# Kernel tuning notes

Hardware: AMD Instinct MI355X
Metric: run time of the kernel (lower is better)

## Reference

```python
import jax, jax.numpy as jnp
import numpy as np

HEADS = 4
DIM_HEAD = 64


def setup_inputs() -> dict:
    key = jax.random.key(0)
    k1, k2, k3, k4 = jax.random.split(key, 4)
    dim = 256
    hidden = HEADS * DIM_HEAD  # 256
    x = jax.random.normal(k1, (16, dim, 64, 64), dtype=jnp.float32)
    # 1x1 conv weights stored as [out_c, in_c]
    w_qkv = jax.random.normal(k2, (3 * hidden, dim), dtype=jnp.float32) * (1.0 / np.sqrt(dim))
    w_out = jax.random.normal(k3, (dim, hidden), dtype=jnp.float32) * (1.0 / np.sqrt(hidden))
    b_out = jax.random.normal(k4, (dim,), dtype=jnp.float32) * 0.01
    gamma = jnp.ones((dim,), dtype=jnp.float32) * 1e-05
    return {"x": x, "w_qkv": w_qkv, "w_out": w_out, "b_out": b_out, "gamma": gamma}


def reference(x, w_qkv, w_out, b_out, gamma):
    b, c, h, w = x.shape
    n = h * w
    # 1x1 conv == channel matmul
    qkv = jnp.einsum('oc,bchw->bohw', w_qkv, x)  # [b, 3*heads*dh, h, w]
    qkv = qkv.reshape(b, 3, HEADS, DIM_HEAD, n)  # channel split order: (qkv, heads, c)
    q, k, v = qkv[:, 0], qkv[:, 1], qkv[:, 2]    # each [b, heads, dh, n]
    k = jax.nn.softmax(k, axis=-1)               # softmax over spatial tokens
    context = jnp.einsum('bhdn,bhen->bhde', k, v)  # [b, heads, dh, dh]
    out = jnp.einsum('bhde,bhdn->bhen', context, q)  # [b, heads, dh, n]
    out = out.reshape(b, HEADS * DIM_HEAD, h, w)
    y = jnp.einsum('oc,bchw->bohw', w_out, out) + b_out[None, :, None, None]
    return y * gamma[None, :, None, None] + x
```

## Files before the change

kernel.cpp:

```cpp
#include <hip/hip_runtime.h>
#include <stdint.h>

typedef short s16x8 __attribute__((ext_vector_type(8)));
typedef float f32x4 __attribute__((ext_vector_type(4)));

__device__ __forceinline__ float bits2f(unsigned short u) {
    union { unsigned int i; float f; } c; c.i = ((unsigned int)u) << 16; return c.f;
}
__device__ __forceinline__ unsigned short f2bits(float f) {
    union { float f; unsigned int i; } c; c.f = f;
    unsigned int x = c.i;
    unsigned int r = (x + 0x7FFFu + ((x >> 16) & 1u)) >> 16;
    return (unsigned short)r;
}
__device__ __forceinline__ unsigned int pack2(float a, float b) {
    return (unsigned int)f2bits(a) | ((unsigned int)f2bits(b) << 16);
}

__global__ __launch_bounds__(256) void k_cvt(
    const float* __restrict__ src, unsigned short* __restrict__ dst, int n8)
{
    int i = blockIdx.x * 256 + threadIdx.x;
    if (i >= n8) return;
    const float* s = src + (size_t)i * 8;
    float4 a = *(const float4*)s, b = *(const float4*)(s + 4);
    unsigned int q[4] = { pack2(a.x, a.y), pack2(a.z, a.w), pack2(b.x, b.y), pack2(b.z, b.w) };
    *(s16x8*)(dst + (size_t)i * 8) = *(s16x8*)q;
}

__global__ __launch_bounds__(256) void k_transpose(
    const unsigned short* __restrict__ src, unsigned short* __restrict__ dst,
    int RS, int DS)
{
    int dr = blockIdx.x * 256 + threadIdx.x;
    int c0 = blockIdx.y * 8;
    __align__(16) unsigned short tmp[8];
#pragma unroll
    for (int j = 0; j < 8; ++j) tmp[j] = src[(size_t)(c0 + j) * RS + dr];
    *(s16x8*)(dst + (size_t)dr * DS + c0) = *(s16x8*)tmp;
}

template <int BF32>
__global__ __launch_bounds__(256) void gemm_bt(
    const unsigned short* __restrict__ A, const void* __restrict__ Bt,
    unsigned short* __restrict__ C,
    int K, int Kstep, int lda, int ldb, int ldc,
    long Abs, long Bbs, long Cbs)
{
    __shared__ unsigned short As[128][72];
    __shared__ unsigned short Bs[128][72];
    int bz = blockIdx.z;
    int b = bz & 15, kc = bz >> 4;
    int m0 = blockIdx.y * 128, n0 = blockIdx.x * 128;
    const unsigned short* Ab = A + (size_t)b * Abs + (size_t)m0 * lda + (size_t)kc * Kstep;
    size_t boff = (size_t)b * Bbs + (size_t)n0 * ldb + (size_t)kc * Kstep;
    int t = threadIdx.x;
    int w = t >> 6, l = t & 63, lm = l & 15, lq = l >> 4;
    int mw = (w >> 1) * 64, nw = (w & 1) * 64;

    f32x4 acc[4][4];
    f32x4 zero = {0.f, 0.f, 0.f, 0.f};
#pragma unroll
    for (int i = 0; i < 4; ++i)
#pragma unroll
        for (int j = 0; j < 4; ++j) acc[i][j] = zero;

    for (int kk = 0; kk < K; kk += 64) {
#pragma unroll
        for (int i = 0; i < 4; ++i) {
            int idx = t + i * 256;
            int r = idx >> 3, ch = idx & 7;
            *(s16x8*)&As[r][ch * 8] = *(const s16x8*)(Ab + (size_t)r * lda + kk + ch * 8);
            if (BF32) {
                const float* bp = (const float*)Bt + boff + (size_t)r * ldb + kk + ch * 8;
                float4 v0 = *(const float4*)bp, v1 = *(const float4*)(bp + 4);
                unsigned int q[4] = { pack2(v0.x, v0.y), pack2(v0.z, v0.w),
                                      pack2(v1.x, v1.y), pack2(v1.z, v1.w) };
                *(s16x8*)&Bs[r][ch * 8] = *(s16x8*)q;
            } else {
                const unsigned short* bp = (const unsigned short*)Bt + boff + (size_t)r * ldb + kk + ch * 8;
                *(s16x8*)&Bs[r][ch * 8] = *(const s16x8*)bp;
            }
        }
        __syncthreads();
#pragma unroll
        for (int ks = 0; ks < 2; ++ks) {
            s16x8 af[4], bfr[4];
#pragma unroll
            for (int mi = 0; mi < 4; ++mi) af[mi]  = *(const s16x8*)&As[mw + mi * 16 + lm][ks * 32 + lq * 8];
#pragma unroll
            for (int ni = 0; ni < 4; ++ni) bfr[ni] = *(const s16x8*)&Bs[nw + ni * 16 + lm][ks * 32 + lq * 8];
#pragma unroll
            for (int mi = 0; mi < 4; ++mi)
#pragma unroll
                for (int ni = 0; ni < 4; ++ni)
                    acc[mi][ni] = __builtin_amdgcn_mfma_f32_16x16x32_bf16(af[mi], bfr[ni], acc[mi][ni], 0, 0, 0);
        }
        __syncthreads();
    }

    unsigned short* Cb = C + (size_t)bz * Cbs;
#pragma unroll
    for (int mi = 0; mi < 4; ++mi)
#pragma unroll
        for (int r = 0; r < 4; ++r) {
            int m = m0 + mw + mi * 16 + lq * 4 + r;
#pragma unroll
            for (int ni = 0; ni < 4; ++ni) {
                int n = n0 + nw + ni * 16 + lm;
                Cb[(size_t)m * ldc + n] = f2bits(acc[mi][ni][r]);
            }
        }
}

template <int EPI>
__global__ __launch_bounds__(256) void gemm_bn(
    const unsigned short* __restrict__ A, const float* __restrict__ B,
    void* __restrict__ C,
    int K, int lda, int ldb, int ldc,
    long Abs, long Bbs, long Cbs,
    const float* __restrict__ Xres,
    const float* __restrict__ gamma,
    const float* __restrict__ bias)
{
    __shared__ unsigned short As[128][72];
    __shared__ unsigned short Bs[64][130];
    int bz = blockIdx.z;
    int m0 = blockIdx.y * 128, n0 = blockIdx.x * 128;
    const unsigned short* Ab = A + (size_t)bz * Abs + (size_t)m0 * lda;
    const float* Bb = B + (size_t)bz * Bbs + n0;
    int t = threadIdx.x;
    int w = t >> 6, l = t & 63, lm = l & 15, lq = l >> 4;
    int mw = (w >> 1) * 64, nw = (w & 1) * 64;

    f32x4 acc[4][4];
    f32x4 zero = {0.f, 0.f, 0.f, 0.f};
#pragma unroll
    for (int i = 0; i < 4; ++i)
#pragma unroll
        for (int j = 0; j < 4; ++j) acc[i][j] = zero;

    for (int kk = 0; kk < K; kk += 64) {
#pragma unroll
        for (int i = 0; i < 4; ++i) {
            int idx = t + i * 256;
            int r = idx >> 3, ch = idx & 7;
            *(s16x8*)&As[r][ch * 8] = *(const s16x8*)(Ab + (size_t)r * lda + kk + ch * 8);
        }
#pragma unroll
        for (int i = 0; i < 4; ++i) {
            int idx = t + i * 256;
            int c = idx >> 4, cc = idx & 15;
            const float* bp = Bb + (size_t)(kk + c) * ldb + cc * 8;
            float4 v0 = *(const float4*)bp, v1 = *(const float4*)(bp + 4);
            unsigned int* q = (unsigned int*)&Bs[c][cc * 8];
            q[0] = pack2(v0.x, v0.y); q[1] = pack2(v0.z, v0.w);
            q[2] = pack2(v1.x, v1.y); q[3] = pack2(v1.z, v1.w);
        }
        __syncthreads();
#pragma unroll
        for (int ks = 0; ks < 2; ++ks) {
            s16x8 af[4];
#pragma unroll
            for (int mi = 0; mi < 4; ++mi) af[mi] = *(const s16x8*)&As[mw + mi * 16 + lm][ks * 32 + lq * 8];
#pragma unroll
            for (int ni = 0; ni < 4; ++ni) {
                s16x8 bfr;
#pragma unroll
                for (int j = 0; j < 8; ++j) bfr[j] = (short)Bs[ks * 32 + lq * 8 + j][nw + ni * 16 + lm];
#pragma unroll
                for (int mi = 0; mi < 4; ++mi)
                    acc[mi][ni] = __builtin_amdgcn_mfma_f32_16x16x32_bf16(af[mi], bfr, acc[mi][ni], 0, 0, 0);
            }
        }
        __syncthreads();
    }

#pragma unroll
    for (int mi = 0; mi < 4; ++mi)
#pragma unroll
        for (int r = 0; r < 4; ++r) {
            int m = m0 + mw + mi * 16 + lq * 4 + r;
            float g = 0.f, bo = 0.f;
            if (EPI == 1) { g = gamma[m]; bo = bias[m]; }
#pragma unroll
            for (int ni = 0; ni < 4; ++ni) {
                int n = n0 + nw + ni * 16 + lm;
                size_t idx = (size_t)m * ldc + n;
                float v = acc[mi][ni][r];
                if (EPI == 1) {
                    float* Cb = (float*)C + (size_t)bz * Cbs;
                    Cb[idx] = g * (v + bo) + Xres[(size_t)bz * Cbs + idx];
                } else {
                    unsigned short* Cb = (unsigned short*)C + (size_t)bz * Cbs;
                    Cb[idx] = f2bits(v);
                }
            }
        }
}

__global__ __launch_bounds__(256) void k_softmax(unsigned short* __restrict__ kbuf)
{
    unsigned short* p = kbuf + (size_t)blockIdx.x * 4096;
    int t = threadIdx.x;
    __shared__ float red[4];

    s16x8 r0 = *(const s16x8*)(p + t * 16);
    s16x8 r1 = *(const s16x8*)(p + t * 16 + 8);
    float v[16];
    float m = -1e30f;
#pragma unroll
    for (int i = 0; i < 8; ++i) { v[i] = bits2f((unsigned short)r0[i]); v[8 + i] = bits2f((unsigned short)r1[i]); }
#pragma unroll
    for (int i = 0; i < 16; ++i) m = fmaxf(m, v[i]);
#pragma unroll
    for (int off = 32; off >= 1; off >>= 1) m = fmaxf(m, __shfl_xor(m, off));
    if ((t & 63) == 0) red[t >> 6] = m;
    __syncthreads();
    m = fmaxf(fmaxf(red[0], red[1]), fmaxf(red[2], red[3]));
    __syncthreads();

    float s = 0.f;
#pragma unroll
    for (int i = 0; i < 16; ++i) { v[i] = __expf(v[i] - m); s += v[i]; }
#pragma unroll
    for (int off = 32; off >= 1; off >>= 1) s += __shfl_xor(s, off);
    if ((t & 63) == 0) red[t >> 6] = s;
    __syncthreads();
    s = red[0] + red[1] + red[2] + red[3];
    float inv = 1.0f / s;

    __align__(16) unsigned short otmp[16];
#pragma unroll
    for (int i = 0; i < 16; ++i) otmp[i] = f2bits(v[i] * inv);
    *(s16x8*)(p + t * 16) = *(s16x8*)(otmp);
    *(s16x8*)(p + t * 16 + 8) = *(s16x8*)(otmp + 8);
}

__global__ __launch_bounds__(256) void k_gred(
    const unsigned short* __restrict__ Gp, unsigned short* __restrict__ G)
{
    int gid = blockIdx.x * 256 + threadIdx.x;
    int b = gid >> 13;
    size_t i8 = (size_t)(gid & 8191) * 8;
    float s[8] = {0.f, 0.f, 0.f, 0.f, 0.f, 0.f, 0.f, 0.f};
#pragma unroll
    for (int kc = 0; kc < 8; ++kc) {
        s16x8 v = *(const s16x8*)(Gp + (size_t)(kc * 16 + b) * 65536 + i8);
#pragma unroll
        for (int j = 0; j < 8; ++j) s[j] += bits2f((unsigned short)v[j]);
    }
    __align__(16) unsigned short tmp[8];
#pragma unroll
    for (int j = 0; j < 8; ++j) tmp[j] = f2bits(s[j]);
    *(s16x8*)(G + (size_t)b * 65536 + i8) = *(s16x8*)tmp;
}

__global__ __launch_bounds__(256) void k_ctxw2(
    const unsigned short* __restrict__ G, const unsigned short* __restrict__ wb,
    const unsigned short* __restrict__ wob, unsigned short* __restrict__ W2)
{
    __shared__ unsigned short ctxs[64][72];
    int h = blockIdx.x, b = blockIdx.y;
    int t = threadIdx.x, w = t >> 6, l = t & 63, lm = l & 15, lq = l >> 4;
    const unsigned short* Gb = G + (size_t)b * 65536 + (size_t)(h * 64) * 256;
    const unsigned short* Wv = wb + 131072 + (size_t)(h * 64) * 256;
    f32x4 zero = {0.f, 0.f, 0.f, 0.f};

    f32x4 acc[4];
#pragma unroll
    for (int i = 0; i < 4; ++i) acc[i] = zero;
    for (int kk = 0; kk < 256; kk += 32) {
        s16x8 a = *(const s16x8*)(Gb + (size_t)(w * 16 + lm) * 256 + kk + lq * 8);
#pragma unroll
        for (int ni = 0; ni < 4; ++ni) {
            s16x8 bb = *(const s16x8*)(Wv + (size_t)(ni * 16 + lm) * 256 + kk + lq * 8);
            acc[ni] = __builtin_amdgcn_mfma_f32_16x16x32_bf16(a, bb, acc[ni], 0, 0, 0);
        }
    }
#pragma unroll
    for (int ni = 0; ni < 4; ++ni)
#pragma unroll
        for (int r = 0; r < 4; ++r)
            ctxs[w * 16 + lq * 4 + r][ni * 16 + lm] = f2bits(acc[ni][r]);
    __syncthreads();

    f32x4 acc2[4][4];
#pragma unroll
    for (int i = 0; i < 4; ++i)
#pragma unroll
        for (int j = 0; j < 4; ++j) acc2[i][j] = zero;
#pragma unroll
    for (int ks = 0; ks < 2; ++ks) {
        s16x8 af[4], bfr[4];
#pragma unroll
        for (int mi = 0; mi < 4; ++mi)
            af[mi] = *(const s16x8*)(wob + (size_t)(w * 64 + mi * 16 + lm) * 256 + h * 64 + ks * 32 + lq * 8);
#pragma unroll
        for (int ni = 0; ni < 4; ++ni) bfr[ni] = *(const s16x8*)&ctxs[ni * 16 + lm][ks * 32 + lq * 8];
#pragma unroll
        for (int mi = 0; mi < 4; ++mi)
#pragma unroll
            for (int ni = 0; ni < 4; ++ni)
                acc2[mi][ni] = __builtin_amdgcn_mfma_f32_16x16x32_bf16(af[mi], bfr[ni], acc2[mi][ni], 0, 0, 0);
    }
    unsigned short* W2b = W2 + (size_t)b * 65536;
#pragma unroll
    for (int mi = 0; mi < 4; ++mi)
#pragma unroll
        for (int r = 0; r < 4; ++r) {
            int o = w * 64 + mi * 16 + lq * 4 + r;
#pragma unroll
            for (int ni = 0; ni < 4; ++ni)
                W2b[(size_t)o * 256 + h * 64 + ni * 16 + lm] = f2bits(acc2[mi][ni][r]);
        }
}

extern "C" void kernel_launch(void* const* d_in, const int* in_sizes, int n_in,
                              void* d_out, int out_size, void* d_ws, size_t ws_size,
                              hipStream_t stream)
{
    (void)in_sizes; (void)n_in; (void)out_size; (void)ws_size;
    const float* x      = (const float*)d_in[0];
    const float* w_qkv  = (const float*)d_in[1];
    const float* w_out  = (const float*)d_in[2];
    const float* b_out  = (const float*)d_in[3];
    const float* gamma  = (const float*)d_in[4];
    unsigned short* kbuf = (unsigned short*)d_out;

    char* ws = (char*)d_ws;
    unsigned short* Gp  = (unsigned short*)(ws);
    unsigned short* G   = (unsigned short*)(ws + 16777216);
    unsigned short* W2  = (unsigned short*)(ws + 18874368);
    unsigned short* W3  = (unsigned short*)(ws + 20971520);
    unsigned short* WqT = (unsigned short*)(ws + 23068672);
    unsigned short* wb  = (unsigned short*)(ws + 23199744);
    unsigned short* wob = (unsigned short*)(ws + 23592960);

    k_cvt<<<dim3(96), 256, 0, stream>>>(w_qkv, wb, 24576);
    k_cvt<<<dim3(32), 256, 0, stream>>>(w_out, wob, 8192);

    k_transpose<<<dim3(1, 32, 1), 256, 0, stream>>>(wb, WqT, 256, 256);

    gemm_bn<0><<<dim3(32, 2, 16), 256, 0, stream>>>(
        wb + 65536, x, kbuf, 256, 256, 4096, 4096,
        0L, 1048576L, 1048576L, nullptr, nullptr, nullptr);

    k_softmax<<<dim3(4096), 256, 0, stream>>>(kbuf);

    gemm_bt<1><<<dim3(2, 2, 128), 256, 0, stream>>>(
        kbuf, x, Gp, 512, 512, 4096, 4096, 256,
        1048576L, 1048576L, 65536L);

    k_gred<<<dim3(512), 256, 0, stream>>>(Gp, G);

    k_ctxw2<<<dim3(4, 16), 256, 0, stream>>>(G, wb, wob, W2);

    gemm_bt<0><<<dim3(2, 2, 16), 256, 0, stream>>>(
        W2, WqT, W3, 256, 0, 256, 256, 256,
        65536L, 0L, 65536L);

    gemm_bn<1><<<dim3(32, 2, 16), 256, 0, stream>>>(
        W3, x, d_out, 256, 256, 4096, 4096,
        65536L, 1048576L, 1048576L, x, gamma, b_out);
}
```

Baseline: 228.7 us.

## Pre-transpose x to bf16 token-major and route big GEMMs through gemm_bt

Adds a prep kernel that converts x to bf16 and transposes it to [n][c] layout in workspace. The K-projection GEMM and the final output GEMM, which has a fused bias, gamma and residual epilogue, now use the B-transposed bf16 GEMM path instead of the fp32 row-major path. The three weight-prep kernels are merged into one launch. Gp moves into the upper half of d_out. This trades an extra 32 MB bf16 write and read of x for cheaper, conversion-free operand loads in two GEMMs, and it depends on a workspace size check, falling back to the old path when the workspace is too small.

```diff
diff --git a/kernel.cpp b/kernel.cpp
--- a/kernel.cpp
+++ b/kernel.cpp
@@ -40,12 +40,68 @@
     *(s16x8*)(dst + (size_t)dr * DS + c0) = *(s16x8*)tmp;
 }
 
-template <int BF32>
+__global__ __launch_bounds__(256) void k_prepw(
+    const float* __restrict__ wqkv, const float* __restrict__ wout,
+    unsigned short* __restrict__ wb, unsigned short* __restrict__ wob,
+    unsigned short* __restrict__ WqT)
+{
+    int i = blockIdx.x * 256 + threadIdx.x;
+    if (i < 32768) {
+        const float* s; unsigned short* d; int j;
+        if (i < 24576) { s = wqkv; d = wb; j = i; }
+        else           { s = wout; d = wob; j = i - 24576; }
+        const float* sp = s + (size_t)j * 8;
+        float4 a = *(const float4*)sp, b = *(const float4*)(sp + 4);
+        unsigned int q[4] = { pack2(a.x, a.y), pack2(a.z, a.w), pack2(b.x, b.y), pack2(b.z, b.w) };
+        *(s16x8*)(d + (size_t)j * 8) = *(s16x8*)q;
+    } else {
+        int j = i - 32768;
+        int dr = j & 255, c0 = (j >> 8) * 8;
+        __align__(16) unsigned short tmp[8];
+#pragma unroll
+        for (int jj = 0; jj < 8; ++jj)
+            tmp[jj] = f2bits(wqkv[(size_t)(c0 + jj) * 256 + dr]);
+        *(s16x8*)(WqT + (size_t)dr * 256 + c0) = *(s16x8*)tmp;
+    }
+}
+
+__global__ __launch_bounds__(256) void k_prep(
+    const float* __restrict__ x, unsigned short* __restrict__ xT)
+{
+    __shared__ unsigned short Ts[64][264];
+    int b = blockIdx.y, n0 = blockIdx.x * 64, t = threadIdx.x;
+    const float* xb = x + (size_t)b * 1048576;
+#pragma unroll
+    for (int i = 0; i < 16; ++i) {
+        int idx = t + i * 256;
+        int c = idx >> 4, nq = idx & 15;
+        float4 v = *(const float4*)(xb + (size_t)c * 4096 + n0 + nq * 4);
+        float vv[4] = { v.x, v.y, v.z, v.w };
+#pragma unroll
+        for (int e = 0; e < 4; ++e) {
+            int ee = (e + c) & 3;
+            Ts[nq * 4 + ee][c] = f2bits(vv[ee]);
+        }
+    }
+    __syncthreads();
+    unsigned short* xTb = xT + (size_t)b * 1048576 + (size_t)n0 * 256;
+#pragma unroll
+    for (int i = 0; i < 8; ++i) {
+        int idx = t + i * 256;
+        int nl = idx >> 5, cg = (idx & 31) * 8;
+        *(s16x8*)(xTb + (size_t)nl * 256 + cg) = *(const s16x8*)&Ts[nl][cg];
+    }
+}
+
+template <int BF32, int EPI>
 __global__ __launch_bounds__(256) void gemm_bt(
     const unsigned short* __restrict__ A, const void* __restrict__ Bt,
-    unsigned short* __restrict__ C,
+    void* __restrict__ C,
     int K, int Kstep, int lda, int ldb, int ldc,
-    long Abs, long Bbs, long Cbs)
+    long Abs, long Bbs, long Cbs,
+    const float* __restrict__ Xres,
+    const float* __restrict__ gamma,
+    const float* __restrict__ bias)
 {
     __shared__ unsigned short As[128][72];
     __shared__ unsigned short Bs[128][72];
@@ -99,18 +155,36 @@
         __syncthreads();
     }
 
-    unsigned short* Cb = C + (size_t)bz * Cbs;
-#pragma unroll
-    for (int mi = 0; mi < 4; ++mi)
-#pragma unroll
-        for (int r = 0; r < 4; ++r) {
-            int m = m0 + mw + mi * 16 + lq * 4 + r;
-#pragma unroll
-            for (int ni = 0; ni < 4; ++ni) {
-                int n = n0 + nw + ni * 16 + lm;
-                Cb[(size_t)m * ldc + n] = f2bits(acc[mi][ni][r]);
+    if (EPI == 0) {
+        unsigned short* Cb = (unsigned short*)C + (size_t)bz * Cbs;
+#pragma unroll
+        for (int mi = 0; mi < 4; ++mi)
+#pragma unroll
+            for (int r = 0; r < 4; ++r) {
+                int m = m0 + mw + mi * 16 + lq * 4 + r;
+#pragma unroll
+                for (int ni = 0; ni < 4; ++ni) {
+                    int n = n0 + nw + ni * 16 + lm;
+                    Cb[(size_t)m * ldc + n] = f2bits(acc[mi][ni][r]);
+                }
             }
-        }
+    } else {
+        float* Cb = (float*)C + (size_t)bz * Cbs;
+        const float* Xb = Xres + (size_t)bz * Cbs;
+#pragma unroll
+        for (int mi = 0; mi < 4; ++mi)
+#pragma unroll
+            for (int r = 0; r < 4; ++r) {
+                int m = m0 + mw + mi * 16 + lq * 4 + r;
+                float g = gamma[m], bo = bias[m];
+#pragma unroll
+                for (int ni = 0; ni < 4; ++ni) {
+                    int n = n0 + nw + ni * 16 + lm;
+                    size_t idx = (size_t)m * ldc + n;
+                    Cb[idx] = g * (acc[mi][ni][r] + bo) + Xb[idx];
+                }
+            }
+    }
 }
 
 template <int EPI>
@@ -320,47 +394,85 @@
                               void* d_out, int out_size, void* d_ws, size_t ws_size,
                               hipStream_t stream)
 {
-    (void)in_sizes; (void)n_in; (void)out_size; (void)ws_size;
+    (void)in_sizes; (void)n_in; (void)out_size;
     const float* x      = (const float*)d_in[0];
     const float* w_qkv  = (const float*)d_in[1];
     const float* w_out  = (const float*)d_in[2];
     const float* b_out  = (const float*)d_in[3];
     const float* gamma  = (const float*)d_in[4];
-    unsigned short* kbuf = (unsigned short*)d_out;
 
     char* ws = (char*)d_ws;
-    unsigned short* Gp  = (unsigned short*)(ws);
-    unsigned short* G   = (unsigned short*)(ws + 16777216);
-    unsigned short* W2  = (unsigned short*)(ws + 18874368);
-    unsigned short* W3  = (unsigned short*)(ws + 20971520);
-    unsigned short* WqT = (unsigned short*)(ws + 23068672);
-    unsigned short* wb  = (unsigned short*)(ws + 23199744);
-    unsigned short* wob = (unsigned short*)(ws + 23592960);
-
-    k_cvt<<<dim3(96), 256, 0, stream>>>(w_qkv, wb, 24576);
-    k_cvt<<<dim3(32), 256, 0, stream>>>(w_out, wob, 8192);
-
-    k_transpose<<<dim3(1, 32, 1), 256, 0, stream>>>(wb, WqT, 256, 256);
-
-    gemm_bn<0><<<dim3(32, 2, 16), 256, 0, stream>>>(
-        wb + 65536, x, kbuf, 256, 256, 4096, 4096,
-        0L, 1048576L, 1048576L, nullptr, nullptr, nullptr);
-
-    k_softmax<<<dim3(4096), 256, 0, stream>>>(kbuf);
-
-    gemm_bt<1><<<dim3(2, 2, 128), 256, 0, stream>>>(
-        kbuf, x, Gp, 512, 512, 4096, 4096, 256,
-        1048576L, 1048576L, 65536L);
-
-    k_gred<<<dim3(512), 256, 0, stream>>>(Gp, G);
-
-    k_ctxw2<<<dim3(4, 16), 256, 0, stream>>>(G, wb, wob, W2);
-
-    gemm_bt<0><<<dim3(2, 2, 16), 256, 0, stream>>>(
-        W2, WqT, W3, 256, 0, 256, 256, 256,
-        65536L, 0L, 65536L);
-
-    gemm_bn<1><<<dim3(32, 2, 16), 256, 0, stream>>>(
-        W3, x, d_out, 256, 256, 4096, 4096,
-        65536L, 1048576L, 1048576L, x, gamma, b_out);
-}
+    const size_t NEED = 40501248;
+
+    if (ws_size >= NEED) {
+        unsigned short* xT  = (unsigned short*)ws;
+        unsigned short* G   = (unsigned short*)(ws + 33554432);
+        unsigned short* W2  = (unsigned short*)(ws + 35651584);
+        unsigned short* W3  = (unsigned short*)(ws + 37748736);
+        unsigned short* WqT = (unsigned short*)(ws + 39845888);
+        unsigned short* wb  = (unsigned short*)(ws + 39976960);
+        unsigned short* wob = (unsigned short*)(ws + 40370176);
+        unsigned short* kbuf = (unsigned short*)d_out;
+        unsigned short* Gp   = (unsigned short*)((char*)d_out + 33554432);
+
+        k_prepw<<<dim3(160), 256, 0, stream>>>(w_qkv, w_out, wb, wob, WqT);
+
+        k_prep<<<dim3(64, 16), 256, 0, stream>>>(x, xT);
+
+        gemm_bt<0, 0><<<dim3(32, 2, 16), 256, 0, stream>>>(
+            wb + 65536, xT, kbuf, 256, 0, 256, 256, 4096,
+            0L, 1048576L, 1048576L, nullptr, nullptr, nullptr);
+
+        k_softmax<<<dim3(4096), 256, 0, stream>>>(kbuf);
+
+        gemm_bt<1, 0><<<dim3(2, 2, 128), 256, 0, stream>>>(
+            kbuf, x, Gp, 512, 512, 4096, 4096, 256,
+            1048576L, 1048576L, 65536L, nullptr, nullptr, nullptr);
+
+        k_gred<<<dim3(512), 256, 0, stream>>>(Gp, G);
+
+        k_ctxw2<<<dim3(4, 16), 256, 0, stream>>>(G, wb, wob, W2);
+
+        gemm_bt<0, 0><<<dim3(2, 2, 16), 256, 0, stream>>>(
+            W2, WqT, W3, 256, 0, 256, 256, 256,
+            65536L, 0L, 65536L, nullptr, nullptr, nullptr);
+
+        gemm_bt<0, 1><<<dim3(32, 2, 16), 256, 0, stream>>>(
+            W3, xT, d_out, 256, 0, 256, 256, 4096,
+            65536L, 1048576L, 1048576L, x, gamma, b_out);
+    } else {
+        unsigned short* kbuf = (unsigned short*)d_out;
+        unsigned short* Gp  = (unsigned short*)(ws);
+        unsigned short* G   = (unsigned short*)(ws + 16777216);
+        unsigned short* W2  = (unsigned short*)(ws + 18874368);
+        unsigned short* W3  = (unsigned short*)(ws + 20971520);
+        unsigned short* WqT = (unsigned short*)(ws + 23068672);
+        unsigned short* wb  = (unsigned short*)(ws + 23199744);
+        unsigned short* wob = (unsigned short*)(ws + 23592960);
+
+        k_cvt<<<dim3(96), 256, 0, stream>>>(w_qkv, wb, 24576);
+        k_cvt<<<dim3(32), 256, 0, stream>>>(w_out, wob, 8192);
+        k_transpose<<<dim3(1, 32, 1), 256, 0, stream>>>(wb, WqT, 256, 256);
+
+        gemm_bn<0><<<dim3(32, 2, 16), 256, 0, stream>>>(
+            wb + 65536, x, kbuf, 256, 256, 4096, 4096,
+            0L, 1048576L, 1048576L, nullptr, nullptr, nullptr);
+
+        k_softmax<<<dim3(4096), 256, 0, stream>>>(kbuf);
+
+        gemm_bt<1, 0><<<dim3(2, 2, 128), 256, 0, stream>>>(
+            kbuf, x, Gp, 512, 512, 4096, 4096, 256,
+            1048576L, 1048576L, 65536L, nullptr, nullptr, nullptr);
+
+        k_gred<<<dim3(512), 256, 0, stream>>>(Gp, G);
+        k_ctxw2<<<dim3(4, 16), 256, 0, stream>>>(G, wb, wob, W2);
+
+        gemm_bt<0, 0><<<dim3(2, 2, 16), 256, 0, stream>>>(
+            W2, WqT, W3, 256, 0, 256, 256, 256,
+            65536L, 0L, 65536L, nullptr, nullptr, nullptr);
+
+        gemm_bn<1><<<dim3(32, 2, 16), 256, 0, stream>>>(
+            W3, x, d_out, 256, 256, 4096, 4096,
+            65536L, 1048576L, 1048576L, x, gamma, b_out);
+    }
+}
```

Result: no change. 232.1 us (+1.5%).
